# Kernel optimization log

Measured on AMD Instinct MI355X. Metric: run time of the kernel, lower is better.

The kernel has to match this reference:

```python
import jax, jax.numpy as jnp
import numpy as np
import math

PRE_NMS_TOP_N = 2000
BBOX_XFORM_CLIP = math.log(1000.0 / 16.0)
TO_REMOVE = 1.0


def _decode(rel_codes, boxes):
    widths = boxes[..., 2] - boxes[..., 0] + TO_REMOVE
    heights = boxes[..., 3] - boxes[..., 1] + TO_REMOVE
    ctr_x = boxes[..., 0] + 0.5 * widths
    ctr_y = boxes[..., 1] + 0.5 * heights

    dx = rel_codes[..., 0]
    dy = rel_codes[..., 1]
    dw = jnp.minimum(rel_codes[..., 2], BBOX_XFORM_CLIP)
    dh = jnp.minimum(rel_codes[..., 3], BBOX_XFORM_CLIP)

    pred_ctr_x = dx * widths + ctr_x
    pred_ctr_y = dy * heights + ctr_y
    pred_w = jnp.exp(dw) * widths
    pred_h = jnp.exp(dh) * heights

    x1 = pred_ctr_x - 0.5 * pred_w
    y1 = pred_ctr_y - 0.5 * pred_h
    x2 = pred_ctr_x + 0.5 * pred_w - 1.0
    y2 = pred_ctr_y + 0.5 * pred_h - 1.0
    return jnp.stack([x1, y1, x2, y2], axis=-1)


def setup_inputs() -> dict:
    key = jax.random.key(0)
    k1, k2, k3 = jax.random.split(key, 3)
    N, A = 8, 500000
    anchors = jax.random.uniform(k1, (N, A, 4), dtype=jnp.float32) * 800.0
    objectness = jax.random.normal(k2, (N, A, 1), dtype=jnp.float32)
    box_regression = jax.random.normal(k3, (N, A, 4), dtype=jnp.float32)
    return {"anchors": anchors, "objectness": objectness, "box_regression": box_regression}


def reference(anchors, objectness, box_regression):
    N, A, _ = objectness.shape
    k = min(PRE_NMS_TOP_N, A)
    scores = objectness[..., 0]                       # [N, A] (C == 1 for RPN)
    top_scores, top_idx = jax.lax.top_k(scores, k)    # sorted descending, [N, k]
    idx = top_idx[..., None]                          # [N, k, 1]
    breg = jnp.take_along_axis(box_regression, idx, axis=1)  # [N, k, 4]
    anc = jnp.take_along_axis(anchors, idx, axis=1)          # [N, k, 4]
    proposals = _decode(breg, anc)                    # [N, k, 4]
    return jnp.concatenate([proposals, top_scores[..., None]], axis=-1)  # [N, k, 5]
```

## Files before the change

### kernel.cpp

```cpp
#include <hip/hip_runtime.h>
#include <stdint.h>
#include <math.h>

#define N_BATCH 8
#define A_ELEMS 500000
#define TOPK    2000
#define NBINS   2048
#define CAP     4096
#define BCAP2   128
#define SBLK    128
#define SEG     16
#define SEGK    256
#define GRP     4
#define BBOX_CLIP 4.135166556742356f

__device__ __forceinline__ uint32_t f2sortable(float f) {
    uint32_t b = __float_as_uint(f);
    return (b & 0x80000000u) ? ~b : (b | 0x80000000u);
}

__global__ __launch_bounds__(256) void scan_kernel(const float* __restrict__ obj,
                                                   uint32_t* __restrict__ bcount,
                                                   unsigned long long* __restrict__ priv) {
    __shared__ uint32_t lcount;
    const int n = blockIdx.y, blk = blockIdx.x;
    const int tid = (int)threadIdx.x;
    if (tid == 0) lcount = 0;
    __syncthreads();
    const uint32_t T0 = f2sortable(2.46f);
    const float4* o4 = (const float4*)(obj + (size_t)n * A_ELEMS);
    unsigned long long* pv = priv + ((size_t)n * SBLK + blk) * BCAP2;
    const int n4 = A_ELEMS / 4;
    for (int i = blk * 256 + tid; i < n4; i += SBLK * 256) {
        float4 v = o4[i];
        uint32_t us[4] = {f2sortable(v.x), f2sortable(v.y), f2sortable(v.z), f2sortable(v.w)};
        #pragma unroll
        for (int c = 0; c < 4; ++c) {
            if (us[c] >= T0) {
                uint32_t pos = atomicAdd(&lcount, 1u);
                if (pos < BCAP2) {
                    uint32_t idx = (uint32_t)(i * 4 + c);
                    pv[pos] = ((unsigned long long)us[c] << 32) |
                              (unsigned long long)(~idx);
                }
            }
        }
    }
    __syncthreads();
    if (tid == 0) bcount[(size_t)n * SBLK + blk] = lcount;
}

__global__ __launch_bounds__(256) void check_kernel(
    const uint32_t* __restrict__ bcount,
    const unsigned long long* __restrict__ priv,
    uint32_t* __restrict__ ok,
    uint32_t* __restrict__ cand_count, unsigned long long* __restrict__ cand) {
    __shared__ uint32_t cs[SBLK];
    __shared__ uint32_t ps[SBLK];
    __shared__ uint32_t pre[SBLK + 1];
    __shared__ uint32_t bad;
    const int n = blockIdx.x;
    const int tid = (int)threadIdx.x;
    if (tid == 0) bad = 0;
    __syncthreads();
    if (tid < SBLK) {
        uint32_t c = bcount[(size_t)n * SBLK + tid];
        cs[tid] = c; ps[tid] = c;
        if (c > BCAP2) atomicOr(&bad, 1u);
    }
    __syncthreads();
    for (int off = 1; off < SBLK; off <<= 1) {
        uint32_t v = 0;
        if (tid < SBLK) { v = ps[tid]; if (tid >= off) v += ps[tid - off]; }
        __syncthreads();
        if (tid < SBLK) ps[tid] = v;
        __syncthreads();
    }
    const uint32_t total = ps[SBLK - 1];
    if (tid < SBLK) pre[tid] = ps[tid] - cs[tid];
    if (tid == 0) pre[SBLK] = total;
    __syncthreads();
    const bool okl = (bad == 0) && (total >= TOPK) && (total <= CAP);
    if (tid == 0) { ok[n] = okl ? 1u : 0u; cand_count[n] = okl ? total : 0u; }
    if (!okl) return;
    const unsigned long long* pv = priv + (size_t)n * SBLK * BCAP2;
    unsigned long long* cn = cand + (size_t)n * CAP;
    for (uint32_t g = tid; g < total; g += 256) {
        int lo = 0, hi = SBLK - 1;
        while (lo < hi) { int mid = (lo + hi + 1) >> 1; if (pre[mid] <= g) lo = mid; else hi = mid - 1; }
        cn[g] = pv[(size_t)lo * BCAP2 + (g - pre[lo])];
    }
}

__global__ __launch_bounds__(256) void repair_kernel(const float* __restrict__ obj,
                               const uint32_t* __restrict__ ok,
                               uint32_t* __restrict__ cand_count,
                               unsigned long long* __restrict__ cand) {
    const int n = blockIdx.x;
    if (ok[n]) return;
    __shared__ uint32_t sh[NBINS];
    __shared__ uint32_t lcount;
    __shared__ uint32_t cutb;
    const int tid = (int)threadIdx.x;
    for (int i = tid; i < NBINS; i += 256) sh[i] = 0;
    if (tid == 0) lcount = 0;
    __syncthreads();
    const float* o = obj + (size_t)n * A_ELEMS;
    for (int i = tid; i < A_ELEMS; i += 256)
        atomicAdd(&sh[f2sortable(o[i]) >> 21], 1u);
    __syncthreads();
    if (tid == 0) {
        uint32_t cum = 0; int b;
        for (b = NBINS - 1; b > 0; --b) { cum += sh[b]; if (cum >= TOPK) break; }
        cutb = (uint32_t)b;
    }
    __syncthreads();
    const uint32_t cb = cutb;
    unsigned long long* cn = cand + (size_t)n * CAP;
    for (int i = tid; i < A_ELEMS; i += 256) {
        uint32_t u = f2sortable(o[i]);
        if ((u >> 21) >= cb) {
            uint32_t pos = atomicAdd(&lcount, 1u);
            if (pos < CAP)
                cn[pos] = ((unsigned long long)u << 32) | (unsigned long long)(~(uint32_t)i);
        }
    }
    __syncthreads();
    if (tid == 0) cand_count[n] = lcount < CAP ? lcount : CAP;
}

__global__ __launch_bounds__(256) void rank_partial_kernel(
    const uint32_t* __restrict__ cand_count,
    const unsigned long long* __restrict__ cand,
    uint16_t* __restrict__ partial) {
    __shared__ unsigned long long s[SEGK];
    const int n = blockIdx.z, seg = blockIdx.y, grp = blockIdx.x;
    uint32_t cnt = cand_count[n];
    if (cnt > CAP) cnt = CAP;
    if ((uint32_t)(grp * 1024) >= cnt) return;
    if ((uint32_t)(seg * SEGK) >= cnt) return;
    const unsigned long long* cn = cand + (size_t)n * CAP;
    const int ks = seg * SEGK;
    for (int i = threadIdx.x; i < SEGK; i += 256)
        s[i] = ((uint32_t)(ks + i) < cnt) ? cn[ks + i] : 0ull;
    __syncthreads();
    const int t0 = grp * 1024 + (int)threadIdx.x;
    unsigned long long k0 = cn[t0], k1 = cn[t0 + 256], k2 = cn[t0 + 512], k3 = cn[t0 + 768];
    uint32_t r0 = 0, r1 = 0, r2 = 0, r3 = 0;
    const ulonglong2* s2 = (const ulonglong2*)s;
    #pragma unroll 8
    for (int j = 0; j < SEGK / 2; ++j) {
        ulonglong2 p = s2[j];
        r0 += (p.x > k0); r0 += (p.y > k0);
        r1 += (p.x > k1); r1 += (p.y > k1);
        r2 += (p.x > k2); r2 += (p.y > k2);
        r3 += (p.x > k3); r3 += (p.y > k3);
    }
    uint16_t* pp = partial + ((size_t)n * SEG + seg) * CAP;
    pp[t0]       = (uint16_t)r0;
    pp[t0 + 256] = (uint16_t)r1;
    pp[t0 + 512] = (uint16_t)r2;
    pp[t0 + 768] = (uint16_t)r3;
}

__global__ __launch_bounds__(256) void decode_kernel(
    const float* __restrict__ anchors, const float* __restrict__ breg,
    const uint32_t* __restrict__ cand_count,
    const unsigned long long* __restrict__ cand,
    const uint16_t* __restrict__ partial,
    float* __restrict__ out) {
    const int n = blockIdx.y;
    const int t = blockIdx.x * 256 + (int)threadIdx.x;
    uint32_t cnt = cand_count[n];
    if (cnt > CAP) cnt = CAP;
    if ((uint32_t)t >= cnt) return;
    const int nseg = (int)((cnt + SEGK - 1) / SEGK);
    const uint16_t* pp = partial + (size_t)n * SEG * CAP;
    uint32_t rank = 0;
    for (int sg = 0; sg < nseg; ++sg) rank += pp[(size_t)sg * CAP + t];
    if (rank >= TOPK) return;
    const unsigned long long mykey = cand[(size_t)n * CAP + t];
    const uint32_t u    = (uint32_t)(mykey >> 32);
    const uint32_t idx  = ~((uint32_t)mykey);
    const uint32_t bits = (u & 0x80000000u) ? (u ^ 0x80000000u) : ~u;
    const float score = __uint_as_float(bits);
    const float4 a = ((const float4*)anchors)[(size_t)n * A_ELEMS + idx];
    const float4 b = ((const float4*)breg)[(size_t)n * A_ELEMS + idx];
    float w  = a.z - a.x + 1.0f;
    float h  = a.w - a.y + 1.0f;
    float cx = a.x + 0.5f * w;
    float cy = a.y + 0.5f * h;
    float dw = fminf(b.z, BBOX_CLIP);
    float dh = fminf(b.w, BBOX_CLIP);
    float pcx = b.x * w + cx;
    float pcy = b.y * h + cy;
    float pw  = expf(dw) * w;
    float ph  = expf(dh) * h;
    float* row = out + ((size_t)n * TOPK + rank) * 5;
    row[0] = pcx - 0.5f * pw;
    row[1] = pcy - 0.5f * ph;
    row[2] = pcx + 0.5f * pw - 1.0f;
    row[3] = pcy + 0.5f * ph - 1.0f;
    row[4] = score;
}

extern "C" void kernel_launch(void* const* d_in, const int* in_sizes, int n_in,
                              void* d_out, int out_size, void* d_ws, size_t ws_size,
                              hipStream_t stream) {
    const float* anchors    = (const float*)d_in[0];
    const float* objectness = (const float*)d_in[1];
    const float* breg       = (const float*)d_in[2];
    float* out = (float*)d_out;

    uint8_t* ws = (uint8_t*)d_ws;
    uint32_t* bcount     = (uint32_t*)ws;
    unsigned long long* priv = (unsigned long long*)(ws + 4096);
    uint32_t* cand_count = (uint32_t*)(ws + 1052672);
    uint32_t* ok         = (uint32_t*)(ws + 1052704);
    unsigned long long* cand = (unsigned long long*)(ws + 1052736);
    uint16_t* partial    = (uint16_t*)(ws + 1314880);

    dim3 g1(SBLK, N_BATCH);
    scan_kernel<<<g1, 256, 0, stream>>>(objectness, bcount, priv);
    check_kernel<<<N_BATCH, 256, 0, stream>>>(bcount, priv, ok, cand_count, cand);
    repair_kernel<<<N_BATCH, 256, 0, stream>>>(objectness, ok, cand_count, cand);
    dim3 g2(GRP, SEG, N_BATCH);
    rank_partial_kernel<<<g2, 256, 0, stream>>>(cand_count, cand, partial);
    dim3 g3(CAP / 256, N_BATCH);
    decode_kernel<<<g3, 256, 0, stream>>>(anchors, breg, cand_count, cand, partial, out);
}
```

Baseline: 160.8 us.

## Fuse scan/check/repair and rank/decode via last-block ticket counters

Merges the scan, check and repair stages into one kernel: the last block to finish for each batch, found with an atomic ticket and thread fences, does the prefix compaction or the histogram fallback. It also merges the rank-partial and decode kernels so that the last segment block of each group does the decode. This cuts five launches to two plus a small memset, removing launch gaps and inter-kernel bubbles. The cost is extra shared memory per scan block, which may reduce occupancy, and a serialized tail on a single block per batch.

```diff
diff --git a/kernel.cpp b/kernel.cpp
--- a/kernel.cpp
+++ b/kernel.cpp
@@ -19,28 +19,42 @@
     return (b & 0x80000000u) ? ~b : (b | 0x80000000u);
 }
 
-__global__ __launch_bounds__(256) void scan_kernel(const float* __restrict__ obj,
-                                                   uint32_t* __restrict__ bcount,
-                                                   unsigned long long* __restrict__ priv) {
+__global__ __launch_bounds__(256) void scan_select_kernel(
+    const float* __restrict__ obj,
+    uint32_t* __restrict__ tick,
+    uint32_t* __restrict__ bcount,
+    unsigned long long* __restrict__ priv,
+    uint32_t* __restrict__ cand_count,
+    unsigned long long* __restrict__ cand)
+{
     __shared__ uint32_t lcount;
+    __shared__ uint32_t lticket;
+    __shared__ uint32_t cs[SBLK];
+    __shared__ uint32_t ps[SBLK];
+    __shared__ uint32_t pre[SBLK + 1];
+    __shared__ uint32_t bad;
+    __shared__ uint32_t cutb;
+    __shared__ uint32_t sh[NBINS];
+
     const int n = blockIdx.y, blk = blockIdx.x;
     const int tid = (int)threadIdx.x;
     if (tid == 0) lcount = 0;
     __syncthreads();
-    const uint32_t T0 = f2sortable(2.46f);
+
+    const float Tf = 2.46f;
     const float4* o4 = (const float4*)(obj + (size_t)n * A_ELEMS);
     unsigned long long* pv = priv + ((size_t)n * SBLK + blk) * BCAP2;
     const int n4 = A_ELEMS / 4;
     for (int i = blk * 256 + tid; i < n4; i += SBLK * 256) {
         float4 v = o4[i];
-        uint32_t us[4] = {f2sortable(v.x), f2sortable(v.y), f2sortable(v.z), f2sortable(v.w)};
+        float fs[4] = {v.x, v.y, v.z, v.w};
         #pragma unroll
         for (int c = 0; c < 4; ++c) {
-            if (us[c] >= T0) {
+            if (fs[c] >= Tf) {
                 uint32_t pos = atomicAdd(&lcount, 1u);
                 if (pos < BCAP2) {
                     uint32_t idx = (uint32_t)(i * 4 + c);
-                    pv[pos] = ((unsigned long long)us[c] << 32) |
+                    pv[pos] = ((unsigned long long)f2sortable(fs[c]) << 32) |
                               (unsigned long long)(~idx);
                 }
             }
@@ -48,19 +62,13 @@
     }
     __syncthreads();
     if (tid == 0) bcount[(size_t)n * SBLK + blk] = lcount;
-}
-
-__global__ __launch_bounds__(256) void check_kernel(
-    const uint32_t* __restrict__ bcount,
-    const unsigned long long* __restrict__ priv,
-    uint32_t* __restrict__ ok,
-    uint32_t* __restrict__ cand_count, unsigned long long* __restrict__ cand) {
-    __shared__ uint32_t cs[SBLK];
-    __shared__ uint32_t ps[SBLK];
-    __shared__ uint32_t pre[SBLK + 1];
-    __shared__ uint32_t bad;
-    const int n = blockIdx.x;
-    const int tid = (int)threadIdx.x;
+    __threadfence();
+    __syncthreads();
+    if (tid == 0) lticket = atomicAdd(&tick[n], 1u);
+    __syncthreads();
+    if (lticket != (uint32_t)(SBLK - 1)) return;
+    __threadfence();
+
     if (tid == 0) bad = 0;
     __syncthreads();
     if (tid < SBLK) {
@@ -81,27 +89,19 @@
     if (tid == 0) pre[SBLK] = total;
     __syncthreads();
     const bool okl = (bad == 0) && (total >= TOPK) && (total <= CAP);
-    if (tid == 0) { ok[n] = okl ? 1u : 0u; cand_count[n] = okl ? total : 0u; }
-    if (!okl) return;
-    const unsigned long long* pv = priv + (size_t)n * SBLK * BCAP2;
     unsigned long long* cn = cand + (size_t)n * CAP;
-    for (uint32_t g = tid; g < total; g += 256) {
-        int lo = 0, hi = SBLK - 1;
-        while (lo < hi) { int mid = (lo + hi + 1) >> 1; if (pre[mid] <= g) lo = mid; else hi = mid - 1; }
-        cn[g] = pv[(size_t)lo * BCAP2 + (g - pre[lo])];
-    }
-}
-
-__global__ __launch_bounds__(256) void repair_kernel(const float* __restrict__ obj,
-                               const uint32_t* __restrict__ ok,
-                               uint32_t* __restrict__ cand_count,
-                               unsigned long long* __restrict__ cand) {
-    const int n = blockIdx.x;
-    if (ok[n]) return;
-    __shared__ uint32_t sh[NBINS];
-    __shared__ uint32_t lcount;
-    __shared__ uint32_t cutb;
-    const int tid = (int)threadIdx.x;
+
+    if (okl) {
+        if (tid == 0) cand_count[n] = total;
+        const unsigned long long* pvb = priv + (size_t)n * SBLK * BCAP2;
+        for (uint32_t g = tid; g < total; g += 256) {
+            int lo = 0, hi = SBLK - 1;
+            while (lo < hi) { int mid = (lo + hi + 1) >> 1; if (pre[mid] <= g) lo = mid; else hi = mid - 1; }
+            cn[g] = pvb[(size_t)lo * BCAP2 + (g - pre[lo])];
+        }
+        return;
+    }
+
     for (int i = tid; i < NBINS; i += 256) sh[i] = 0;
     if (tid == 0) lcount = 0;
     __syncthreads();
@@ -116,7 +116,6 @@
     }
     __syncthreads();
     const uint32_t cb = cutb;
-    unsigned long long* cn = cand + (size_t)n * CAP;
     for (int i = tid; i < A_ELEMS; i += 256) {
         uint32_t u = f2sortable(o[i]);
         if ((u >> 21) >= cb) {
@@ -129,79 +128,83 @@
     if (tid == 0) cand_count[n] = lcount < CAP ? lcount : CAP;
 }
 
-__global__ __launch_bounds__(256) void rank_partial_kernel(
+__global__ __launch_bounds__(256) void rank_decode_kernel(
+    const float* __restrict__ anchors, const float* __restrict__ breg,
+    uint32_t* __restrict__ tick,
     const uint32_t* __restrict__ cand_count,
     const unsigned long long* __restrict__ cand,
-    uint16_t* __restrict__ partial) {
+    uint16_t* __restrict__ partial,
+    float* __restrict__ out)
+{
     __shared__ unsigned long long s[SEGK];
+    __shared__ uint32_t lticket;
     const int n = blockIdx.z, seg = blockIdx.y, grp = blockIdx.x;
+    const int tid = (int)threadIdx.x;
     uint32_t cnt = cand_count[n];
     if (cnt > CAP) cnt = CAP;
-    if ((uint32_t)(grp * 1024) >= cnt) return;
-    if ((uint32_t)(seg * SEGK) >= cnt) return;
     const unsigned long long* cn = cand + (size_t)n * CAP;
-    const int ks = seg * SEGK;
-    for (int i = threadIdx.x; i < SEGK; i += 256)
-        s[i] = ((uint32_t)(ks + i) < cnt) ? cn[ks + i] : 0ull;
-    __syncthreads();
-    const int t0 = grp * 1024 + (int)threadIdx.x;
-    unsigned long long k0 = cn[t0], k1 = cn[t0 + 256], k2 = cn[t0 + 512], k3 = cn[t0 + 768];
-    uint32_t r0 = 0, r1 = 0, r2 = 0, r3 = 0;
-    const ulonglong2* s2 = (const ulonglong2*)s;
-    #pragma unroll 8
-    for (int j = 0; j < SEGK / 2; ++j) {
-        ulonglong2 p = s2[j];
-        r0 += (p.x > k0); r0 += (p.y > k0);
-        r1 += (p.x > k1); r1 += (p.y > k1);
-        r2 += (p.x > k2); r2 += (p.y > k2);
-        r3 += (p.x > k3); r3 += (p.y > k3);
-    }
-    uint16_t* pp = partial + ((size_t)n * SEG + seg) * CAP;
-    pp[t0]       = (uint16_t)r0;
-    pp[t0 + 256] = (uint16_t)r1;
-    pp[t0 + 512] = (uint16_t)r2;
-    pp[t0 + 768] = (uint16_t)r3;
-}
-
-__global__ __launch_bounds__(256) void decode_kernel(
-    const float* __restrict__ anchors, const float* __restrict__ breg,
-    const uint32_t* __restrict__ cand_count,
-    const unsigned long long* __restrict__ cand,
-    const uint16_t* __restrict__ partial,
-    float* __restrict__ out) {
-    const int n = blockIdx.y;
-    const int t = blockIdx.x * 256 + (int)threadIdx.x;
-    uint32_t cnt = cand_count[n];
-    if (cnt > CAP) cnt = CAP;
-    if ((uint32_t)t >= cnt) return;
+    const bool live = ((uint32_t)(grp * 1024) < cnt) && ((uint32_t)(seg * SEGK) < cnt);
+    if (live) {
+        const int ks = seg * SEGK;
+        for (int i = tid; i < SEGK; i += 256)
+            s[i] = ((uint32_t)(ks + i) < cnt) ? cn[ks + i] : 0ull;
+        __syncthreads();
+        const int t0 = grp * 1024 + tid;
+        unsigned long long k0 = cn[t0], k1 = cn[t0 + 256], k2 = cn[t0 + 512], k3 = cn[t0 + 768];
+        uint32_t r0 = 0, r1 = 0, r2 = 0, r3 = 0;
+        const ulonglong2* s2 = (const ulonglong2*)s;
+        #pragma unroll 8
+        for (int j = 0; j < SEGK / 2; ++j) {
+            ulonglong2 p = s2[j];
+            r0 += (p.x > k0); r0 += (p.y > k0);
+            r1 += (p.x > k1); r1 += (p.y > k1);
+            r2 += (p.x > k2); r2 += (p.y > k2);
+            r3 += (p.x > k3); r3 += (p.y > k3);
+        }
+        uint16_t* pw = partial + ((size_t)n * SEG + seg) * CAP;
+        pw[t0]       = (uint16_t)r0;
+        pw[t0 + 256] = (uint16_t)r1;
+        pw[t0 + 512] = (uint16_t)r2;
+        pw[t0 + 768] = (uint16_t)r3;
+    }
+    __threadfence();
+    __syncthreads();
+    if (tid == 0) lticket = atomicAdd(&tick[(size_t)n * GRP + grp], 1u);
+    __syncthreads();
+    if (lticket != (uint32_t)(SEG - 1)) return;
+    __threadfence();
+
     const int nseg = (int)((cnt + SEGK - 1) / SEGK);
     const uint16_t* pp = partial + (size_t)n * SEG * CAP;
-    uint32_t rank = 0;
-    for (int sg = 0; sg < nseg; ++sg) rank += pp[(size_t)sg * CAP + t];
-    if (rank >= TOPK) return;
-    const unsigned long long mykey = cand[(size_t)n * CAP + t];
-    const uint32_t u    = (uint32_t)(mykey >> 32);
-    const uint32_t idx  = ~((uint32_t)mykey);
-    const uint32_t bits = (u & 0x80000000u) ? (u ^ 0x80000000u) : ~u;
-    const float score = __uint_as_float(bits);
-    const float4 a = ((const float4*)anchors)[(size_t)n * A_ELEMS + idx];
-    const float4 b = ((const float4*)breg)[(size_t)n * A_ELEMS + idx];
-    float w  = a.z - a.x + 1.0f;
-    float h  = a.w - a.y + 1.0f;
-    float cx = a.x + 0.5f * w;
-    float cy = a.y + 0.5f * h;
-    float dw = fminf(b.z, BBOX_CLIP);
-    float dh = fminf(b.w, BBOX_CLIP);
-    float pcx = b.x * w + cx;
-    float pcy = b.y * h + cy;
-    float pw  = expf(dw) * w;
-    float ph  = expf(dh) * h;
-    float* row = out + ((size_t)n * TOPK + rank) * 5;
-    row[0] = pcx - 0.5f * pw;
-    row[1] = pcy - 0.5f * ph;
-    row[2] = pcx + 0.5f * pw - 1.0f;
-    row[3] = pcy + 0.5f * ph - 1.0f;
-    row[4] = score;
+    for (int t = grp * 1024 + tid; t < grp * 1024 + 1024; t += 256) {
+        if ((uint32_t)t >= cnt) break;
+        uint32_t rank = 0;
+        for (int sg = 0; sg < nseg; ++sg) rank += pp[(size_t)sg * CAP + t];
+        if (rank >= TOPK) continue;
+        const unsigned long long mykey = cn[t];
+        const uint32_t u    = (uint32_t)(mykey >> 32);
+        const uint32_t idx  = ~((uint32_t)mykey);
+        const uint32_t bits = (u & 0x80000000u) ? (u ^ 0x80000000u) : ~u;
+        const float score = __uint_as_float(bits);
+        const float4 a = ((const float4*)anchors)[(size_t)n * A_ELEMS + idx];
+        const float4 b = ((const float4*)breg)[(size_t)n * A_ELEMS + idx];
+        float w  = a.z - a.x + 1.0f;
+        float h  = a.w - a.y + 1.0f;
+        float cx = a.x + 0.5f * w;
+        float cy = a.y + 0.5f * h;
+        float dw = fminf(b.z, BBOX_CLIP);
+        float dh = fminf(b.w, BBOX_CLIP);
+        float pcx = b.x * w + cx;
+        float pcy = b.y * h + cy;
+        float pw  = expf(dw) * w;
+        float ph  = expf(dh) * h;
+        float* row = out + ((size_t)n * TOPK + rank) * 5;
+        row[0] = pcx - 0.5f * pw;
+        row[1] = pcy - 0.5f * ph;
+        row[2] = pcx + 0.5f * pw - 1.0f;
+        row[3] = pcy + 0.5f * ph - 1.0f;
+        row[4] = score;
+    }
 }
 
 extern "C" void kernel_launch(void* const* d_in, const int* in_sizes, int n_in,
@@ -213,19 +216,19 @@
     float* out = (float*)d_out;
 
     uint8_t* ws = (uint8_t*)d_ws;
-    uint32_t* bcount     = (uint32_t*)ws;
-    unsigned long long* priv = (unsigned long long*)(ws + 4096);
-    uint32_t* cand_count = (uint32_t*)(ws + 1052672);
-    uint32_t* ok         = (uint32_t*)(ws + 1052704);
-    unsigned long long* cand = (unsigned long long*)(ws + 1052736);
-    uint16_t* partial    = (uint16_t*)(ws + 1314880);
-
+    uint32_t* tick1      = (uint32_t*)ws;
+    uint32_t* tick2      = (uint32_t*)(ws + 32);
+    uint32_t* bcount     = (uint32_t*)(ws + 256);
+    unsigned long long* priv = (unsigned long long*)(ws + 8192);
+    uint32_t* cand_count = (uint32_t*)(ws + 1056768);
+    unsigned long long* cand = (unsigned long long*)(ws + 1056800);
+    uint16_t* partial    = (uint16_t*)(ws + 1318944);
+
+    hipMemsetAsync(ws, 0, 256, stream);
     dim3 g1(SBLK, N_BATCH);
-    scan_kernel<<<g1, 256, 0, stream>>>(objectness, bcount, priv);
-    check_kernel<<<N_BATCH, 256, 0, stream>>>(bcount, priv, ok, cand_count, cand);
-    repair_kernel<<<N_BATCH, 256, 0, stream>>>(objectness, ok, cand_count, cand);
+    scan_select_kernel<<<g1, 256, 0, stream>>>(objectness, tick1, bcount, priv,
+                                               cand_count, cand);
     dim3 g2(GRP, SEG, N_BATCH);
-    rank_partial_kernel<<<g2, 256, 0, stream>>>(cand_count, cand, partial);
-    dim3 g3(CAP / 256, N_BATCH);
-    decode_kernel<<<g3, 256, 0, stream>>>(anchors, breg, cand_count, cand, partial, out);
-}
+    rank_decode_kernel<<<g2, 256, 0, stream>>>(anchors, breg, tick2, cand_count,
+                                               cand, partial, out);
+}
```

Result: slower. 288.1 us (+79.1%).

## Fuse compaction and repair stages into rank and decode kernels

Applied to the files above, without the earlier changes.

Removes the check and repair kernels. Each rank and decode block rebuilds the per-block prefix sum and gathers keys from the private scan buffers by binary search, instead of reading a compacted candidate array. The histogram fallback moves into the decode kernel with a brute-force rank. This cuts two launches and a global compaction pass, at the cost of redundant prefix scans per block and a slow fallback path.

```diff
diff --git a/kernel.cpp b/kernel.cpp
--- a/kernel.cpp
+++ b/kernel.cpp
@@ -12,11 +12,20 @@
 #define SEG     16
 #define SEGK    256
 #define GRP     4
+#define FBCAP   8192
 #define BBOX_CLIP 4.135166556742356f
+
 
 __device__ __forceinline__ uint32_t f2sortable(float f) {
     uint32_t b = __float_as_uint(f);
     return (b & 0x80000000u) ? ~b : (b | 0x80000000u);
+}
+
+__device__ __forceinline__ unsigned long long gather_key(
+    const unsigned long long* pvb, const uint32_t* pre, uint32_t g) {
+    int lo = 0, hi = SBLK - 1;
+    while (lo < hi) { int mid = (lo + hi + 1) >> 1; if (pre[mid] <= g) lo = mid; else hi = mid - 1; }
+    return pvb[(size_t)lo * BCAP2 + (g - pre[lo])];
 }
 
 __global__ __launch_bounds__(256) void scan_kernel(const float* __restrict__ obj,
@@ -27,20 +36,20 @@
     const int tid = (int)threadIdx.x;
     if (tid == 0) lcount = 0;
     __syncthreads();
-    const uint32_t T0 = f2sortable(2.46f);
+    const float Tf = 2.46f;
     const float4* o4 = (const float4*)(obj + (size_t)n * A_ELEMS);
     unsigned long long* pv = priv + ((size_t)n * SBLK + blk) * BCAP2;
     const int n4 = A_ELEMS / 4;
     for (int i = blk * 256 + tid; i < n4; i += SBLK * 256) {
         float4 v = o4[i];
-        uint32_t us[4] = {f2sortable(v.x), f2sortable(v.y), f2sortable(v.z), f2sortable(v.w)};
+        float fs[4] = {v.x, v.y, v.z, v.w};
         #pragma unroll
         for (int c = 0; c < 4; ++c) {
-            if (us[c] >= T0) {
+            if (fs[c] >= Tf) {
                 uint32_t pos = atomicAdd(&lcount, 1u);
                 if (pos < BCAP2) {
                     uint32_t idx = (uint32_t)(i * 4 + c);
-                    pv[pos] = ((unsigned long long)us[c] << 32) |
+                    pv[pos] = ((unsigned long long)f2sortable(fs[c]) << 32) |
                               (unsigned long long)(~idx);
                 }
             }
@@ -50,23 +59,15 @@
     if (tid == 0) bcount[(size_t)n * SBLK + blk] = lcount;
 }
 
-__global__ __launch_bounds__(256) void check_kernel(
-    const uint32_t* __restrict__ bcount,
-    const unsigned long long* __restrict__ priv,
-    uint32_t* __restrict__ ok,
-    uint32_t* __restrict__ cand_count, unsigned long long* __restrict__ cand) {
-    __shared__ uint32_t cs[SBLK];
-    __shared__ uint32_t ps[SBLK];
-    __shared__ uint32_t pre[SBLK + 1];
-    __shared__ uint32_t bad;
-    const int n = blockIdx.x;
-    const int tid = (int)threadIdx.x;
-    if (tid == 0) bad = 0;
+__device__ __forceinline__ uint32_t build_prefix(
+    const uint32_t* bcount, int n, int tid,
+    uint32_t* cs, uint32_t* ps, uint32_t* pre, uint32_t* bad) {
+    if (tid == 0) *bad = 0;
     __syncthreads();
     if (tid < SBLK) {
         uint32_t c = bcount[(size_t)n * SBLK + tid];
         cs[tid] = c; ps[tid] = c;
-        if (c > BCAP2) atomicOr(&bad, 1u);
+        if (c > BCAP2) atomicOr(bad, 1u);
     }
     __syncthreads();
     for (int off = 1; off < SBLK; off <<= 1) {
@@ -80,72 +81,34 @@
     if (tid < SBLK) pre[tid] = ps[tid] - cs[tid];
     if (tid == 0) pre[SBLK] = total;
     __syncthreads();
-    const bool okl = (bad == 0) && (total >= TOPK) && (total <= CAP);
-    if (tid == 0) { ok[n] = okl ? 1u : 0u; cand_count[n] = okl ? total : 0u; }
-    if (!okl) return;
-    const unsigned long long* pv = priv + (size_t)n * SBLK * BCAP2;
-    unsigned long long* cn = cand + (size_t)n * CAP;
-    for (uint32_t g = tid; g < total; g += 256) {
-        int lo = 0, hi = SBLK - 1;
-        while (lo < hi) { int mid = (lo + hi + 1) >> 1; if (pre[mid] <= g) lo = mid; else hi = mid - 1; }
-        cn[g] = pv[(size_t)lo * BCAP2 + (g - pre[lo])];
-    }
-}
-
-__global__ __launch_bounds__(256) void repair_kernel(const float* __restrict__ obj,
-                               const uint32_t* __restrict__ ok,
-                               uint32_t* __restrict__ cand_count,
-                               unsigned long long* __restrict__ cand) {
-    const int n = blockIdx.x;
-    if (ok[n]) return;
-    __shared__ uint32_t sh[NBINS];
-    __shared__ uint32_t lcount;
-    __shared__ uint32_t cutb;
-    const int tid = (int)threadIdx.x;
-    for (int i = tid; i < NBINS; i += 256) sh[i] = 0;
-    if (tid == 0) lcount = 0;
-    __syncthreads();
-    const float* o = obj + (size_t)n * A_ELEMS;
-    for (int i = tid; i < A_ELEMS; i += 256)
-        atomicAdd(&sh[f2sortable(o[i]) >> 21], 1u);
-    __syncthreads();
-    if (tid == 0) {
-        uint32_t cum = 0; int b;
-        for (b = NBINS - 1; b > 0; --b) { cum += sh[b]; if (cum >= TOPK) break; }
-        cutb = (uint32_t)b;
-    }
-    __syncthreads();
-    const uint32_t cb = cutb;
-    unsigned long long* cn = cand + (size_t)n * CAP;
-    for (int i = tid; i < A_ELEMS; i += 256) {
-        uint32_t u = f2sortable(o[i]);
-        if ((u >> 21) >= cb) {
-            uint32_t pos = atomicAdd(&lcount, 1u);
-            if (pos < CAP)
-                cn[pos] = ((unsigned long long)u << 32) | (unsigned long long)(~(uint32_t)i);
-        }
-    }
-    __syncthreads();
-    if (tid == 0) cand_count[n] = lcount < CAP ? lcount : CAP;
+    return total;
 }
 
 __global__ __launch_bounds__(256) void rank_partial_kernel(
-    const uint32_t* __restrict__ cand_count,
-    const unsigned long long* __restrict__ cand,
+    const uint32_t* __restrict__ bcount,
+    const unsigned long long* __restrict__ priv,
     uint16_t* __restrict__ partial) {
     __shared__ unsigned long long s[SEGK];
+    __shared__ uint32_t cs[SBLK], ps[SBLK], pre[SBLK + 1], bad;
     const int n = blockIdx.z, seg = blockIdx.y, grp = blockIdx.x;
-    uint32_t cnt = cand_count[n];
-    if (cnt > CAP) cnt = CAP;
+    const int tid = (int)threadIdx.x;
+    const uint32_t total = build_prefix(bcount, n, tid, cs, ps, pre, &bad);
+    const bool okl = (bad == 0) && (total >= TOPK) && (total <= CAP);
+    if (!okl) return;
+    const uint32_t cnt = total;
     if ((uint32_t)(grp * 1024) >= cnt) return;
     if ((uint32_t)(seg * SEGK) >= cnt) return;
-    const unsigned long long* cn = cand + (size_t)n * CAP;
+    const unsigned long long* pvb = priv + (size_t)n * SBLK * BCAP2;
     const int ks = seg * SEGK;
-    for (int i = threadIdx.x; i < SEGK; i += 256)
-        s[i] = ((uint32_t)(ks + i) < cnt) ? cn[ks + i] : 0ull;
-    __syncthreads();
-    const int t0 = grp * 1024 + (int)threadIdx.x;
-    unsigned long long k0 = cn[t0], k1 = cn[t0 + 256], k2 = cn[t0 + 512], k3 = cn[t0 + 768];
+    for (int i = tid; i < SEGK; i += 256)
+        s[i] = ((uint32_t)(ks + i) < cnt) ? gather_key(pvb, pre, ks + i) : 0ull;
+    const uint32_t t0 = (uint32_t)(grp * 1024 + tid);
+    const uint32_t cm = cnt - 1;
+    unsigned long long k0 = gather_key(pvb, pre, t0 < cm ? t0 : cm);
+    unsigned long long k1 = gather_key(pvb, pre, t0 + 256 < cm ? t0 + 256 : cm);
+    unsigned long long k2 = gather_key(pvb, pre, t0 + 512 < cm ? t0 + 512 : cm);
+    unsigned long long k3 = gather_key(pvb, pre, t0 + 768 < cm ? t0 + 768 : cm);
+    __syncthreads();
     uint32_t r0 = 0, r1 = 0, r2 = 0, r3 = 0;
     const ulonglong2* s2 = (const ulonglong2*)s;
     #pragma unroll 8
@@ -156,52 +119,118 @@
         r2 += (p.x > k2); r2 += (p.y > k2);
         r3 += (p.x > k3); r3 += (p.y > k3);
     }
-    uint16_t* pp = partial + ((size_t)n * SEG + seg) * CAP;
-    pp[t0]       = (uint16_t)r0;
-    pp[t0 + 256] = (uint16_t)r1;
-    pp[t0 + 512] = (uint16_t)r2;
-    pp[t0 + 768] = (uint16_t)r3;
+    uint16_t* pw = partial + ((size_t)n * SEG + seg) * CAP;
+    pw[t0]       = (uint16_t)r0;
+    pw[t0 + 256] = (uint16_t)r1;
+    pw[t0 + 512] = (uint16_t)r2;
+    pw[t0 + 768] = (uint16_t)r3;
 }
 
 __global__ __launch_bounds__(256) void decode_kernel(
     const float* __restrict__ anchors, const float* __restrict__ breg,
-    const uint32_t* __restrict__ cand_count,
-    const unsigned long long* __restrict__ cand,
+    const float* __restrict__ obj,
+    const uint32_t* __restrict__ bcount,
+    unsigned long long* __restrict__ priv,
     const uint16_t* __restrict__ partial,
     float* __restrict__ out) {
+    __shared__ uint32_t cs[SBLK], ps[SBLK], pre[SBLK + 1], bad;
+    __shared__ uint32_t sh[NBINS];
+    __shared__ uint32_t lcnt, cutb;
     const int n = blockIdx.y;
-    const int t = blockIdx.x * 256 + (int)threadIdx.x;
-    uint32_t cnt = cand_count[n];
-    if (cnt > CAP) cnt = CAP;
-    if ((uint32_t)t >= cnt) return;
-    const int nseg = (int)((cnt + SEGK - 1) / SEGK);
-    const uint16_t* pp = partial + (size_t)n * SEG * CAP;
-    uint32_t rank = 0;
-    for (int sg = 0; sg < nseg; ++sg) rank += pp[(size_t)sg * CAP + t];
-    if (rank >= TOPK) return;
-    const unsigned long long mykey = cand[(size_t)n * CAP + t];
-    const uint32_t u    = (uint32_t)(mykey >> 32);
-    const uint32_t idx  = ~((uint32_t)mykey);
-    const uint32_t bits = (u & 0x80000000u) ? (u ^ 0x80000000u) : ~u;
-    const float score = __uint_as_float(bits);
-    const float4 a = ((const float4*)anchors)[(size_t)n * A_ELEMS + idx];
-    const float4 b = ((const float4*)breg)[(size_t)n * A_ELEMS + idx];
-    float w  = a.z - a.x + 1.0f;
-    float h  = a.w - a.y + 1.0f;
-    float cx = a.x + 0.5f * w;
-    float cy = a.y + 0.5f * h;
-    float dw = fminf(b.z, BBOX_CLIP);
-    float dh = fminf(b.w, BBOX_CLIP);
-    float pcx = b.x * w + cx;
-    float pcy = b.y * h + cy;
-    float pw  = expf(dw) * w;
-    float ph  = expf(dh) * h;
-    float* row = out + ((size_t)n * TOPK + rank) * 5;
-    row[0] = pcx - 0.5f * pw;
-    row[1] = pcy - 0.5f * ph;
-    row[2] = pcx + 0.5f * pw - 1.0f;
-    row[3] = pcy + 0.5f * ph - 1.0f;
-    row[4] = score;
+    const int tid = (int)threadIdx.x;
+    const uint32_t total = build_prefix(bcount, n, tid, cs, ps, pre, &bad);
+    const bool okl = (bad == 0) && (total >= TOPK) && (total <= CAP);
+
+    if (okl) {
+        const uint32_t cnt = total;
+        const uint32_t t = (uint32_t)(blockIdx.x * 256 + tid);
+        if (t >= cnt) return;
+        const int nseg = (int)((cnt + SEGK - 1) / SEGK);
+        const uint16_t* pp = partial + (size_t)n * SEG * CAP;
+        uint32_t rank = 0;
+        for (int sg = 0; sg < nseg; ++sg) rank += pp[(size_t)sg * CAP + t];
+        if (rank >= TOPK) return;
+        const unsigned long long* pvb = priv + (size_t)n * SBLK * BCAP2;
+        const unsigned long long mykey = gather_key(pvb, pre, t);
+        const uint32_t u    = (uint32_t)(mykey >> 32);
+        const uint32_t idx  = ~((uint32_t)mykey);
+        const uint32_t bits = (u & 0x80000000u) ? (u ^ 0x80000000u) : ~u;
+        const float score = __uint_as_float(bits);
+        const float4 a = ((const float4*)anchors)[(size_t)n * A_ELEMS + idx];
+        const float4 b = ((const float4*)breg)[(size_t)n * A_ELEMS + idx];
+        float w  = a.z - a.x + 1.0f;
+        float h  = a.w - a.y + 1.0f;
+        float cx = a.x + 0.5f * w;
+        float cy = a.y + 0.5f * h;
+        float dw = fminf(b.z, BBOX_CLIP);
+        float dh = fminf(b.w, BBOX_CLIP);
+        float pcx = b.x * w + cx;
+        float pcy = b.y * h + cy;
+        float pw  = expf(dw) * w;
+        float ph  = expf(dh) * h;
+        float* row = out + ((size_t)n * TOPK + rank) * 5;
+        row[0] = pcx - 0.5f * pw;
+        row[1] = pcy - 0.5f * ph;
+        row[2] = pcx + 0.5f * pw - 1.0f;
+        row[3] = pcy + 0.5f * ph - 1.0f;
+        row[4] = score;
+        return;
+    }
+
+    if (blockIdx.x != 0) return;
+    for (int i = tid; i < NBINS; i += 256) sh[i] = 0;
+    if (tid == 0) lcnt = 0;
+    __syncthreads();
+    const float* o = obj + (size_t)n * A_ELEMS;
+    for (int i = tid; i < A_ELEMS; i += 256)
+        atomicAdd(&sh[f2sortable(o[i]) >> 21], 1u);
+    __syncthreads();
+    if (tid == 0) {
+        uint32_t cum = 0; int b;
+        for (b = NBINS - 1; b > 0; --b) { cum += sh[b]; if (cum >= TOPK) break; }
+        cutb = (uint32_t)b;
+    }
+    __syncthreads();
+    const uint32_t cb = cutb;
+    unsigned long long* fbn = priv + (size_t)n * SBLK * BCAP2;
+    for (int i = tid; i < A_ELEMS; i += 256) {
+        uint32_t u = f2sortable(o[i]);
+        if ((u >> 21) >= cb) {
+            uint32_t pos = atomicAdd(&lcnt, 1u);
+            if (pos < FBCAP)
+                fbn[pos] = ((unsigned long long)u << 32) | (unsigned long long)(~(uint32_t)i);
+        }
+    }
+    __syncthreads();
+    const uint32_t cnt2 = lcnt < FBCAP ? lcnt : FBCAP;
+    for (uint32_t t = tid; t < cnt2; t += 256) {
+        const unsigned long long myk = fbn[t];
+        uint32_t rank = 0;
+        for (uint32_t j = 0; j < cnt2; ++j) rank += (fbn[j] > myk);
+        if (rank >= TOPK) continue;
+        const uint32_t u    = (uint32_t)(myk >> 32);
+        const uint32_t idx  = ~((uint32_t)myk);
+        const uint32_t bits = (u & 0x80000000u) ? (u ^ 0x80000000u) : ~u;
+        const float score = __uint_as_float(bits);
+        const float4 a = ((const float4*)anchors)[(size_t)n * A_ELEMS + idx];
+        const float4 b = ((const float4*)breg)[(size_t)n * A_ELEMS + idx];
+        float w  = a.z - a.x + 1.0f;
+        float h  = a.w - a.y + 1.0f;
+        float cx = a.x + 0.5f * w;
+        float cy = a.y + 0.5f * h;
+        float dw = fminf(b.z, BBOX_CLIP);
+        float dh = fminf(b.w, BBOX_CLIP);
+        float pcx = b.x * w + cx;
+        float pcy = b.y * h + cy;
+        float pw  = expf(dw) * w;
+        float ph  = expf(dh) * h;
+        float* row = out + ((size_t)n * TOPK + rank) * 5;
+        row[0] = pcx - 0.5f * pw;
+        row[1] = pcy - 0.5f * ph;
+        row[2] = pcx + 0.5f * pw - 1.0f;
+        row[3] = pcy + 0.5f * ph - 1.0f;
+        row[4] = score;
+    }
 }
 
 extern "C" void kernel_launch(void* const* d_in, const int* in_sizes, int n_in,
@@ -213,19 +242,15 @@
     float* out = (float*)d_out;
 
     uint8_t* ws = (uint8_t*)d_ws;
-    uint32_t* bcount     = (uint32_t*)ws;
+    uint32_t* bcount         = (uint32_t*)ws;
     unsigned long long* priv = (unsigned long long*)(ws + 4096);
-    uint32_t* cand_count = (uint32_t*)(ws + 1052672);
-    uint32_t* ok         = (uint32_t*)(ws + 1052704);
-    unsigned long long* cand = (unsigned long long*)(ws + 1052736);
-    uint16_t* partial    = (uint16_t*)(ws + 1314880);
+    uint16_t* partial        = (uint16_t*)(ws + 1052672);
 
     dim3 g1(SBLK, N_BATCH);
     scan_kernel<<<g1, 256, 0, stream>>>(objectness, bcount, priv);
-    check_kernel<<<N_BATCH, 256, 0, stream>>>(bcount, priv, ok, cand_count, cand);
-    repair_kernel<<<N_BATCH, 256, 0, stream>>>(objectness, ok, cand_count, cand);
     dim3 g2(GRP, SEG, N_BATCH);
-    rank_partial_kernel<<<g2, 256, 0, stream>>>(cand_count, cand, partial);
+    rank_partial_kernel<<<g2, 256, 0, stream>>>(bcount, priv, partial);
     dim3 g3(CAP / 256, N_BATCH);
-    decode_kernel<<<g3, 256, 0, stream>>>(anchors, breg, cand_count, cand, partial, out);
-}
+    decode_kernel<<<g3, 256, 0, stream>>>(anchors, breg, objectness, bcount, priv,
+                                          partial, out);
+}
```

Result: faster. 149.5 us, median of 2 (-7.0%).
